# Performance work log

Measured on AMD Instinct MI355X. Metric: run time of the kernel, lower is better.

The kernel has to match this reference:

```python
import jax, jax.numpy as jnp
import numpy as np

D = 128      # embedding_dim
E = 50000    # positive edges per metapath
S = 16       # negative samples per edge
N_A = 100000 # nodes of type A (head type of both metapaths)
N_B = 50000  # nodes of type B (tail type of metapath 1)


def setup_inputs() -> dict:
    key = jax.random.key(0)
    ks = jax.random.split(key, 10)
    emb_A = jax.random.normal(ks[0], (N_A, D), dtype=jnp.float32)
    emb_B = jax.random.normal(ks[1], (N_B, D), dtype=jnp.float32)
    # nn.init.uniform_(a=-1, b=1)
    rel_emb = jax.random.uniform(ks[2], (2, D, D), dtype=jnp.float32, minval=-1.0, maxval=1.0)
    edge_index_m0 = jax.random.randint(ks[3], (2, E), 0, N_A)  # A -> A
    edge_index_m1 = jnp.stack([
        jax.random.randint(ks[4], (E,), 0, N_A),               # heads: type A
        jax.random.randint(ks[5], (E,), 0, N_B),               # tails: type B
    ])
    neg_head_m0 = jax.random.randint(ks[6], (E, S), 0, N_A)
    neg_head_m1 = jax.random.randint(ks[7], (E, S), 0, N_A)
    neg_tail_m0 = jax.random.randint(ks[8], (E, S), 0, N_A)
    neg_tail_m1 = jax.random.randint(ks[9], (E, S), 0, N_B)
    return dict(emb_A=emb_A, emb_B=emb_B, rel_emb=rel_emb,
                edge_index_m0=edge_index_m0, edge_index_m1=edge_index_m1,
                neg_head_m0=neg_head_m0, neg_head_m1=neg_head_m1,
                neg_tail_m0=neg_tail_m0, neg_tail_m1=neg_tail_m1)


# The torch module computes score = (A K B^T).sum(dim=1); summing the [E,E]
# score matrix over dim 1 equals contracting with sum_j b_j, so we never
# materialize the [E,E] (or [E*S, E*S]) matrix -- same math, fused reduction.

def _pos_score(K, emb_h, emb_t, edge_index):
    s = emb_t[edge_index[1]].sum(0)          # [d] = sum_j b_j
    return emb_h[edge_index[0]] @ (K @ s)    # [E]


def _neg_head_score(K, emb_h, neg):
    # predict(mode='head'): emb_A = emb_h[neg.reshape(-1)],
    # idx_B = edge_index[0][arange(E)*S] == neg[:, 0],
    # side_B = (K @ emb_h[idx_B].T).repeat_interleave(S, -1); sum over columns
    # == K @ (S * sum_j emb_h[neg[j, 0]]).
    s = neg.shape[1]
    c = K @ (s * emb_h[neg[:, 0]].sum(0))    # [d]
    return emb_h[neg.reshape(-1)] @ c        # [E*S]


def _neg_tail_score(K, emb_t, neg):
    # predict(mode='tail'): emb_B = emb_t[neg.reshape(-1)],
    # idx_A = edge_index[1][arange(E)*S] == neg[:, 0],
    # side_A = (emb_t[idx_A] @ K).repeat_interleave(S, 0); row sums of
    # side_A @ emb_B^T == side_A @ sum_j emb_B[j].
    s = neg.shape[1]
    sb = emb_t[neg.reshape(-1)].sum(0)       # [d]
    base = (emb_t[neg[:, 0]] @ K) @ sb       # [E]
    return jnp.repeat(base, s)               # [E*S]


def reference(emb_A, emb_B, rel_emb, edge_index_m0, edge_index_m1,
              neg_head_m0, neg_head_m1, neg_tail_m0, neg_tail_m1):
    K0, K1 = rel_emb[0], rel_emb[1]
    pos0 = _pos_score(K0, emb_A, emb_A, edge_index_m0)   # [E]
    pos1 = _pos_score(K1, emb_A, emb_B, edge_index_m1)   # [E]
    nh0 = _neg_head_score(K0, emb_A, neg_head_m0)        # [E*S]
    nh1 = _neg_head_score(K1, emb_A, neg_head_m1)        # [E*S]
    nt0 = _neg_tail_score(K0, emb_A, neg_tail_m0)        # [E*S]
    nt1 = _neg_tail_score(K1, emb_B, neg_tail_m1)        # [E*S]
    return jnp.concatenate([pos0, pos1, nh0, nh1, nt0, nt1])
```

## Files before the change

### kernel.cpp

```cpp
#include <hip/hip_runtime.h>
#include <stdint.h>

#define D 128
#define E_EDGES 50000
#define S_NEG 16
#define N_A 100000
#define N_B 50000
#define ES (E_EDGES * S_NEG)

#define HW 12500
#define ACH 38
#define BCH 34
#define GA 1024
#define GB 512
#define RPG 13
#define RA 32
#define RB 16

__device__ inline float dot4(float4 a, float4 b) {
    return a.x * b.x + a.y * b.y + a.z * b.z + a.w * b.w;
}
#define RED32(p) { p += __shfl_xor(p, 1); p += __shfl_xor(p, 2); p += __shfl_xor(p, 4); \
                   p += __shfl_xor(p, 8); p += __shfl_xor(p, 16); }


__global__ void k_hist(const int* __restrict__ ei0, const int* __restrict__ ei1,
                       const int* __restrict__ nh0, const int* __restrict__ nh1,
                       const int* __restrict__ nt0, const int* __restrict__ nt1,
                       uint32_t* __restrict__ partA, uint32_t* __restrict__ partB) {
    __shared__ uint32_t h[HW];
    const int tid = threadIdx.x;
    for (int w = tid; w < HW; w += 512) h[w] = 0;
    __syncthreads();

    const int b = blockIdx.x;
    if (b < 2 * ACH) {
        const int c = b >> 1, hh = b & 1;
        const unsigned lo = hh * 50000u;
        uint32_t* dst = partA + (size_t)b * HW;
        if (c >= 2 && c < 6) {
            const int* src = (c < 4) ? nh0 : nh1;
            const long long base = (long long)(c & 1) * 25000 * S_NEG;
            for (int i = tid; i < 25000; i += 512) {
                const unsigned r = (unsigned)src[base + (long long)i * S_NEG] - lo;
                if (r < 50000u) atomicAdd(&h[r >> 2], 1u << ((r & 3u) * 8u));
            }
        } else {
            const int* srcp = (c < 2) ? (ei0 + E_EDGES + c * 25000)
                                      : (nt0 + (c - 6) * 25000);
            const int4* src4 = reinterpret_cast<const int4*>(srcp);
            for (int i = tid; i < 6250; i += 512) {
                const int4 v = src4[i];
                unsigned r;
                r = (unsigned)v.x - lo; if (r < 50000u) atomicAdd(&h[r >> 2], 1u << ((r & 3u) * 8u));
                r = (unsigned)v.y - lo; if (r < 50000u) atomicAdd(&h[r >> 2], 1u << ((r & 3u) * 8u));
                r = (unsigned)v.z - lo; if (r < 50000u) atomicAdd(&h[r >> 2], 1u << ((r & 3u) * 8u));
                r = (unsigned)v.w - lo; if (r < 50000u) atomicAdd(&h[r >> 2], 1u << ((r & 3u) * 8u));
            }
        }
        __syncthreads();
        for (int w = tid; w < HW; w += 512) dst[w] = h[w];
    } else {
        const int c = b - 2 * ACH;
        uint32_t* dst = partB + (size_t)c * HW;
        const int* srcp = (c < 2) ? (ei1 + E_EDGES + c * 25000)
                                  : (nt1 + (c - 2) * 25000);
        const int4* src4 = reinterpret_cast<const int4*>(srcp);
        for (int i = tid; i < 6250; i += 512) {
            const int4 v = src4[i];
            unsigned r;
            r = (unsigned)v.x; if (r < 50000u) atomicAdd(&h[r >> 2], 1u << ((r & 3u) * 8u));
            r = (unsigned)v.y; if (r < 50000u) atomicAdd(&h[r >> 2], 1u << ((r & 3u) * 8u));
            r = (unsigned)v.z; if (r < 50000u) atomicAdd(&h[r >> 2], 1u << ((r & 3u) * 8u));
            r = (unsigned)v.w; if (r < 50000u) atomicAdd(&h[r >> 2], 1u << ((r & 3u) * 8u));
        }
        __syncthreads();
        for (int w = tid; w < HW; w += 512) dst[w] = h[w];
    }
}

__global__ void k_reduceC(const uint32_t* __restrict__ partA,
                          const uint32_t* __restrict__ partB,
                          float4* __restrict__ cwA, float2* __restrict__ cwB) {
    const int t = blockIdx.x * 256 + threadIdx.x;
    if (t < N_A) {
        const int n = t;
        const int hh = (n >= 50000);
        const int w = (n - hh * 50000) >> 2;
        const int sh = (n & 3) * 8;
        const uint32_t* p = partA + (size_t)hh * HW + w;
        unsigned s0 = 0, s1 = 0, s2 = 0, s3 = 0;
#pragma unroll
        for (int c = 0; c < 2; ++c)  s0 += (p[(size_t)(c * 2) * HW] >> sh) & 255u;
#pragma unroll
        for (int c = 2; c < 4; ++c)  s1 += (p[(size_t)(c * 2) * HW] >> sh) & 255u;
#pragma unroll
        for (int c = 4; c < 6; ++c)  s2 += (p[(size_t)(c * 2) * HW] >> sh) & 255u;
#pragma unroll 8
        for (int c = 6; c < 38; ++c) s3 += (p[(size_t)(c * 2) * HW] >> sh) & 255u;
        cwA[n] = make_float4((float)s0, (float)s1, (float)s2, (float)s3);
    } else if (t < N_A + N_B) {
        const int n = t - N_A;
        const int w = n >> 2;
        const int sh = (n & 3) * 8;
        const uint32_t* p = partB + w;
        unsigned s0 = 0, s1 = 0;
#pragma unroll
        for (int c = 0; c < 2; ++c)  s0 += (p[(size_t)c * HW] >> sh) & 255u;
#pragma unroll 8
        for (int c = 2; c < 34; ++c) s1 += (p[(size_t)c * HW] >> sh) & 255u;
        cwB[n] = make_float2((float)s0, (float)s1);
    }
}

__global__ void k_scan1(const float* __restrict__ embA, const float* __restrict__ embB,
                        const float4* __restrict__ cwA, const float2* __restrict__ cwB,
                        float* __restrict__ psumA, float* __restrict__ psumB) {
    __shared__ float sds[4 * D];
    const int tid = threadIdx.x;
    const int l = tid & 31;
    const int grp = tid >> 5;

    for (int j = tid; j < 4 * D; j += 256) sds[j] = 0.f;
    __syncthreads();

    if ((int)blockIdx.x < GA) {
        const int gid = blockIdx.x * 8 + grp;
        int r = gid * RPG;
        const int end = min(r + RPG, N_A);
        float acc[16];
#pragma unroll
        for (int k = 0; k < 16; ++k) acc[k] = 0.f;
        const float* base = embA + 4 * l;
        for (; r + 4 <= end; r += 4) {
            float4 w[4], x[4];
#pragma unroll
            for (int u = 0; u < 4; ++u) w[u] = cwA[r + u];
#pragma unroll
            for (int u = 0; u < 4; ++u)
                x[u] = *reinterpret_cast<const float4*>(base + (size_t)(r + u) * D);
#pragma unroll
            for (int u = 0; u < 4; ++u) {
                acc[0]  += w[u].x * x[u].x; acc[1]  += w[u].x * x[u].y;
                acc[2]  += w[u].x * x[u].z; acc[3]  += w[u].x * x[u].w;
                acc[4]  += w[u].y * x[u].x; acc[5]  += w[u].y * x[u].y;
                acc[6]  += w[u].y * x[u].z; acc[7]  += w[u].y * x[u].w;
                acc[8]  += w[u].z * x[u].x; acc[9]  += w[u].z * x[u].y;
                acc[10] += w[u].z * x[u].z; acc[11] += w[u].z * x[u].w;
                acc[12] += w[u].w * x[u].x; acc[13] += w[u].w * x[u].y;
                acc[14] += w[u].w * x[u].z; acc[15] += w[u].w * x[u].w;
            }
        }
        for (; r < end; ++r) {
            const float4 w0 = cwA[r];
            const float4 x0 = *reinterpret_cast<const float4*>(base + (size_t)r * D);
            acc[0]  += w0.x * x0.x; acc[1]  += w0.x * x0.y; acc[2]  += w0.x * x0.z; acc[3]  += w0.x * x0.w;
            acc[4]  += w0.y * x0.x; acc[5]  += w0.y * x0.y; acc[6]  += w0.y * x0.z; acc[7]  += w0.y * x0.w;
            acc[8]  += w0.z * x0.x; acc[9]  += w0.z * x0.y; acc[10] += w0.z * x0.z; acc[11] += w0.z * x0.w;
            acc[12] += w0.w * x0.x; acc[13] += w0.w * x0.y; acc[14] += w0.w * x0.z; acc[15] += w0.w * x0.w;
        }
#pragma unroll
        for (int p = 0; p < 4; ++p)
#pragma unroll
            for (int k = 0; k < 4; ++k)
                atomicAdd(&sds[p * D + 4 * l + k], acc[p * 4 + k]);
        __syncthreads();
        for (int j = tid; j < 4 * D; j += 256)
            psumA[(size_t)blockIdx.x * 512 + j] = sds[j];
    } else {
        const int gid = (blockIdx.x - GA) * 8 + grp;
        int r = gid * RPG;
        const int end = min(r + RPG, N_B);
        float acc[8];
#pragma unroll
        for (int k = 0; k < 8; ++k) acc[k] = 0.f;
        const float* base = embB + 4 * l;
        for (; r + 4 <= end; r += 4) {
            float2 w[4]; float4 x[4];
#pragma unroll
            for (int u = 0; u < 4; ++u) w[u] = cwB[r + u];
#pragma unroll
            for (int u = 0; u < 4; ++u)
                x[u] = *reinterpret_cast<const float4*>(base + (size_t)(r + u) * D);
#pragma unroll
            for (int u = 0; u < 4; ++u) {
                acc[0] += w[u].x * x[u].x; acc[1] += w[u].x * x[u].y;
                acc[2] += w[u].x * x[u].z; acc[3] += w[u].x * x[u].w;
                acc[4] += w[u].y * x[u].x; acc[5] += w[u].y * x[u].y;
                acc[6] += w[u].y * x[u].z; acc[7] += w[u].y * x[u].w;
            }
        }
        for (; r < end; ++r) {
            const float2 w0 = cwB[r];
            const float4 x0 = *reinterpret_cast<const float4*>(base + (size_t)r * D);
            acc[0] += w0.x * x0.x; acc[1] += w0.x * x0.y; acc[2] += w0.x * x0.z; acc[3] += w0.x * x0.w;
            acc[4] += w0.y * x0.x; acc[5] += w0.y * x0.y; acc[6] += w0.y * x0.z; acc[7] += w0.y * x0.w;
        }
#pragma unroll
        for (int p = 0; p < 2; ++p)
#pragma unroll
            for (int k = 0; k < 4; ++k)
                atomicAdd(&sds[p * D + 4 * l + k], acc[p * 4 + k]);
        __syncthreads();
        for (int j = tid; j < 2 * D; j += 256)
            psumB[(size_t)(blockIdx.x - GA) * 256 + j] = sds[j];
    }
}

__global__ void k_red1(const float* __restrict__ psumA, const float* __restrict__ psumB,
                       float* __restrict__ psumA2, float* __restrict__ psumB2) {
    const int b = blockIdx.x, t = threadIdx.x;
    if (b < RA) {
        const float* p = psumA + (size_t)b * 32 * 512;
        float s0 = 0.f, s1 = 0.f;
#pragma unroll 8
        for (int r = 0; r < 32; ++r) { s0 += p[r * 512 + t]; s1 += p[r * 512 + 256 + t]; }
        psumA2[(size_t)b * 512 + t] = s0;
        psumA2[(size_t)b * 512 + 256 + t] = s1;
    } else {
        const int bi = b - RA;
        const float* p = psumB + (size_t)bi * 32 * 256;
        float s = 0.f;
#pragma unroll 8
        for (int r = 0; r < 32; ++r) s += p[r * 256 + t];
        psumB2[(size_t)bi * 256 + t] = s;
    }
}

__global__ void k_cvec2(const float* __restrict__ rel,
                        const float* __restrict__ psumA2, const float* __restrict__ psumB2,
                        float* __restrict__ cvec) {
    const int j = blockIdx.x;
    const int tid = threadIdx.x;
    __shared__ float Kds[D * 129];
    __shared__ float red[256];
    __shared__ float sv[D];
    const float* Kp = rel + (size_t)(j & 1) * D * D;

    for (int e = tid; e < D * D / 4; e += 256) {
        const int row = e >> 5, col = (e & 31) * 4;
        const float4 v = *reinterpret_cast<const float4*>(Kp + (size_t)row * D + col);
        float* dst = Kds + row * 129 + col;
        dst[0] = v.x; dst[1] = v.y; dst[2] = v.z; dst[3] = v.w;
    }

    const int g = tid >> 7, i = tid & 127;
    float s = 0.f;
    if (j == 1 || j == 5) {
        const int plane = (j == 1) ? 0 : 1;
        for (int b = g; b < RB; b += 2) s += psumB2[(size_t)b * 256 + plane * D + i];
    } else {
        const int plane = (j == 0) ? 0 : (j - 1);
        for (int b = g; b < RA; b += 2) s += psumA2[(size_t)b * 512 + plane * D + i];
    }
    red[tid] = s;
    __syncthreads();
    if (tid < 128) sv[i] = red[i] + red[128 + i];
    __syncthreads();

    if (tid < 128) {
        const float scale = (j == 2 || j == 3) ? (float)S_NEG : 1.0f;
        float acc = 0.f;
#pragma unroll
        for (int k = 0; k < D; k += 4)
            acc += Kds[i * 129 + k] * sv[k] + Kds[i * 129 + k + 1] * sv[k + 1]
                 + Kds[i * 129 + k + 2] * sv[k + 2] + Kds[i * 129 + k + 3] * sv[k + 3];
        cvec[j * D + i] = acc * scale;
    }
}

__global__ void k_scan2(const float* __restrict__ embA, const float* __restrict__ embB,
                        const float* __restrict__ cvec, float* __restrict__ PA,
                        float* __restrict__ PB) {
    __shared__ float sc[5 * D];
    const int tid = threadIdx.x;
    const int l = tid & 31;
    const int grp = tid >> 5;

    if ((int)blockIdx.x < GA) {
        for (int j = tid; j < 5 * D; j += 256) sc[j] = cvec[j];
        __syncthreads();
        float4 cf[5];
#pragma unroll
        for (int p = 0; p < 5; ++p)
            cf[p] = *reinterpret_cast<const float4*>(sc + p * D + 4 * l);
        const int gid = blockIdx.x * 8 + grp;
        int r = gid * RPG;
        const int end = min(r + RPG, N_A);
        const float* base = embA + 4 * l;
        for (; r + 4 <= end; r += 4) {
            float4 x[4];
#pragma unroll
            for (int u = 0; u < 4; ++u)
                x[u] = *reinterpret_cast<const float4*>(base + (size_t)(r + u) * D);
            float p_[4][5];
#pragma unroll
            for (int u = 0; u < 4; ++u)
#pragma unroll
                for (int p = 0; p < 5; ++p) p_[u][p] = dot4(x[u], cf[p]);
#pragma unroll
            for (int u = 0; u < 4; ++u)
#pragma unroll
                for (int p = 0; p < 5; ++p) RED32(p_[u][p]);
            if (l < 4) {
#pragma unroll
                for (int p = 0; p < 5; ++p) {
                    float v = p_[0][p];
                    v = (l == 1) ? p_[1][p] : v;
                    v = (l == 2) ? p_[2][p] : v;
                    v = (l == 3) ? p_[3][p] : v;
                    PA[(size_t)p * N_A + r + l] = v;
                }
            }
        }
        for (; r < end; ++r) {
            const float4 x0 = *reinterpret_cast<const float4*>(base + (size_t)r * D);
            float q[5];
#pragma unroll
            for (int p = 0; p < 5; ++p) { q[p] = dot4(x0, cf[p]); RED32(q[p]); }
            if (l == 0) {
#pragma unroll
                for (int p = 0; p < 5; ++p) PA[(size_t)p * N_A + r] = q[p];
            }
        }
    } else {
        for (int j = tid; j < D; j += 256) sc[j] = cvec[5 * D + j];
        __syncthreads();
        const float4 cf = *reinterpret_cast<const float4*>(sc + 4 * l);
        const int gid = (blockIdx.x - GA) * 8 + grp;
        int r = gid * RPG;
        const int end = min(r + RPG, N_B);
        const float* base = embB + 4 * l;
        for (; r + 4 <= end; r += 4) {
            float4 x[4];
#pragma unroll
            for (int u = 0; u < 4; ++u)
                x[u] = *reinterpret_cast<const float4*>(base + (size_t)(r + u) * D);
            float p_[4];
#pragma unroll
            for (int u = 0; u < 4; ++u) { p_[u] = dot4(x[u], cf); RED32(p_[u]); }
            if (l < 4)
                PB[r + l] = (l == 1) ? p_[1] : (l == 2) ? p_[2] : (l == 3) ? p_[3] : p_[0];
        }
        for (; r < end; ++r) {
            const float4 x0 = *reinterpret_cast<const float4*>(base + (size_t)r * D);
            float q = dot4(x0, cf); RED32(q);
            if (l == 0) PB[r] = q;
        }
    }
}

__global__ void k_scatter(const int* __restrict__ ei0, const int* __restrict__ ei1,
                          const int* __restrict__ nh0, const int* __restrict__ nh1,
                          const int* __restrict__ nt0, const int* __restrict__ nt1,
                          const float* __restrict__ PA, const float* __restrict__ PB,
                          float* __restrict__ out) {
    const int total4 = (2 * E_EDGES + 4 * ES) / 4;
    const float* P0 = PA;
    const float* P1 = PA + (size_t)N_A;
    const float* P2 = PA + (size_t)2 * N_A;
    const float* P3 = PA + (size_t)3 * N_A;
    const float* P4 = PA + (size_t)4 * N_A;
    for (int t = blockIdx.x * blockDim.x + threadIdx.x; t < total4;
         t += gridDim.x * blockDim.x) {
        const int e = t * 4;
        float4 v;
        if (e < E_EDGES) {
            const int4 i4 = *reinterpret_cast<const int4*>(ei0 + e);
            v = make_float4(P0[i4.x], P0[i4.y], P0[i4.z], P0[i4.w]);
        } else if (e < 2 * E_EDGES) {
            const int4 i4 = *reinterpret_cast<const int4*>(ei1 + (e - E_EDGES));
            v = make_float4(P1[i4.x], P1[i4.y], P1[i4.z], P1[i4.w]);
        } else if (e < 2 * E_EDGES + ES) {
            const int4 i4 = *reinterpret_cast<const int4*>(nh0 + (e - 2 * E_EDGES));
            v = make_float4(P2[i4.x], P2[i4.y], P2[i4.z], P2[i4.w]);
        } else if (e < 2 * E_EDGES + 2 * ES) {
            const int4 i4 = *reinterpret_cast<const int4*>(nh1 + (e - 2 * E_EDGES - ES));
            v = make_float4(P3[i4.x], P3[i4.y], P3[i4.z], P3[i4.w]);
        } else if (e < 2 * E_EDGES + 3 * ES) {
            const int i = e - 2 * E_EDGES - 2 * ES;
            const float s = P4[nt0[(i >> 4) << 4]];
            v = make_float4(s, s, s, s);
        } else {
            const int i = e - 2 * E_EDGES - 3 * ES;
            const float s = PB[nt1[(i >> 4) << 4]];
            v = make_float4(s, s, s, s);
        }
        *reinterpret_cast<float4*>(out + e) = v;
    }
}

extern "C" void kernel_launch(void* const* d_in, const int* in_sizes, int n_in,
                              void* d_out, int out_size, void* d_ws, size_t ws_size,
                              hipStream_t stream) {
    const float* embA = (const float*)d_in[0];
    const float* embB = (const float*)d_in[1];
    const float* rel  = (const float*)d_in[2];
    const int* ei0 = (const int*)d_in[3];
    const int* ei1 = (const int*)d_in[4];
    const int* nh0 = (const int*)d_in[5];
    const int* nh1 = (const int*)d_in[6];
    const int* nt0 = (const int*)d_in[7];
    const int* nt1 = (const int*)d_in[8];
    float* out = (float*)d_out;

    uint32_t* partA = (uint32_t*)d_ws;
    uint32_t* partB = partA + (size_t)2 * ACH * HW;
    float4* cwA = (float4*)(partB + (size_t)BCH * HW);
    float2* cwB = (float2*)(cwA + N_A);
    float* psumA = (float*)(cwB + N_B);
    float* psumB = psumA + (size_t)GA * 512;
    float* psumA2 = psumB + (size_t)GB * 256;
    float* psumB2 = psumA2 + (size_t)RA * 512;
    float* cvec  = psumB2 + (size_t)RB * 256;
    float* PA    = cvec + 6 * D;
    float* PB    = PA + (size_t)5 * N_A;

    k_hist<<<2 * ACH + BCH, 512, 0, stream>>>(ei0, ei1, nh0, nh1, nt0, nt1, partA, partB);
    k_reduceC<<<(N_A + N_B + 255) / 256, 256, 0, stream>>>(partA, partB, cwA, cwB);
    k_scan1<<<GA + GB, 256, 0, stream>>>(embA, embB, cwA, cwB, psumA, psumB);
    k_red1<<<RA + RB, 256, 0, stream>>>(psumA, psumB, psumA2, psumB2);
    k_cvec2<<<6, 256, 0, stream>>>(rel, psumA2, psumB2, cvec);
    k_scan2<<<GA + GB, 256, 0, stream>>>(embA, embB, cvec, PA, PB);
    k_scatter<<<2048, 256, 0, stream>>>(ei0, ei1, nh0, nh1, nt0, nt1, PA, PB, out);
}
```

Baseline: 227.4 us.

## Restructure embedding scans: exact row partitioning, prefetching, thread-per-row projection

```diff
diff --git a/kernel.cpp b/kernel.cpp
--- a/kernel.cpp
+++ b/kernel.cpp
@@ -11,17 +11,28 @@
 #define HW 12500
 #define ACH 38
 #define BCH 34
-#define GA 1024
-#define GB 512
-#define RPG 13
-#define RA 32
-#define RB 16
+
+#define GA1 500
+#define GB1 250
+#define RPG 25
+#define RA2 20
+#define RB2 10
+#define GA2 391
+#define GB2 196
 
 __device__ inline float dot4(float4 a, float4 b) {
     return a.x * b.x + a.y * b.y + a.z * b.z + a.w * b.w;
 }
-#define RED32(p) { p += __shfl_xor(p, 1); p += __shfl_xor(p, 2); p += __shfl_xor(p, 4); \
-                   p += __shfl_xor(p, 8); p += __shfl_xor(p, 16); }
+__device__ inline void fma16(float* acc, const float4 w, const float4 x) {
+    acc[0]  += w.x * x.x; acc[1]  += w.x * x.y; acc[2]  += w.x * x.z; acc[3]  += w.x * x.w;
+    acc[4]  += w.y * x.x; acc[5]  += w.y * x.y; acc[6]  += w.y * x.z; acc[7]  += w.y * x.w;
+    acc[8]  += w.z * x.x; acc[9]  += w.z * x.y; acc[10] += w.z * x.z; acc[11] += w.z * x.w;
+    acc[12] += w.w * x.x; acc[13] += w.w * x.y; acc[14] += w.w * x.z; acc[15] += w.w * x.w;
+}
+__device__ inline void fma8(float* acc, const float2 w, const float4 x) {
+    acc[0] += w.x * x.x; acc[1] += w.x * x.y; acc[2] += w.x * x.z; acc[3] += w.x * x.w;
+    acc[4] += w.y * x.x; acc[5] += w.y * x.y; acc[6] += w.y * x.z; acc[7] += w.y * x.w;
+}
 
 
 __global__ void k_hist(const int* __restrict__ ei0, const int* __restrict__ ei1,
@@ -113,116 +124,121 @@
     }
 }
 
-__global__ void k_scan1(const float* __restrict__ embA, const float* __restrict__ embB,
-                        const float4* __restrict__ cwA, const float2* __restrict__ cwB,
-                        float* __restrict__ psumA, float* __restrict__ psumB) {
-    __shared__ float sds[4 * D];
+__global__ void __launch_bounds__(256, 4)
+k_scan1(const float* __restrict__ embA, const float* __restrict__ embB,
+        const float4* __restrict__ cwA, const float2* __restrict__ cwB,
+        float* __restrict__ psumA, float* __restrict__ psumB) {
+    __shared__ float sds[4 * 512];
     const int tid = threadIdx.x;
     const int l = tid & 31;
     const int grp = tid >> 5;
-
-    for (int j = tid; j < 4 * D; j += 256) sds[j] = 0.f;
-    __syncthreads();
-
-    if ((int)blockIdx.x < GA) {
-        const int gid = blockIdx.x * 8 + grp;
-        int r = gid * RPG;
-        const int end = min(r + RPG, N_A);
+    const int wid = tid >> 6;
+
+    if ((int)blockIdx.x < GA1) {
+        const int r0 = (blockIdx.x * 8 + grp) * RPG;
+        const float* base = embA + 4 * l;
         float acc[16];
 #pragma unroll
         for (int k = 0; k < 16; ++k) acc[k] = 0.f;
-        const float* base = embA + 4 * l;
-        for (; r + 4 <= end; r += 4) {
-            float4 w[4], x[4];
-#pragma unroll
-            for (int u = 0; u < 4; ++u) w[u] = cwA[r + u];
-#pragma unroll
-            for (int u = 0; u < 4; ++u)
-                x[u] = *reinterpret_cast<const float4*>(base + (size_t)(r + u) * D);
-#pragma unroll
-            for (int u = 0; u < 4; ++u) {
-                acc[0]  += w[u].x * x[u].x; acc[1]  += w[u].x * x[u].y;
-                acc[2]  += w[u].x * x[u].z; acc[3]  += w[u].x * x[u].w;
-                acc[4]  += w[u].y * x[u].x; acc[5]  += w[u].y * x[u].y;
-                acc[6]  += w[u].y * x[u].z; acc[7]  += w[u].y * x[u].w;
-                acc[8]  += w[u].z * x[u].x; acc[9]  += w[u].z * x[u].y;
-                acc[10] += w[u].z * x[u].z; acc[11] += w[u].z * x[u].w;
-                acc[12] += w[u].w * x[u].x; acc[13] += w[u].w * x[u].y;
-                acc[14] += w[u].w * x[u].z; acc[15] += w[u].w * x[u].w;
-            }
-        }
-        for (; r < end; ++r) {
-            const float4 w0 = cwA[r];
-            const float4 x0 = *reinterpret_cast<const float4*>(base + (size_t)r * D);
-            acc[0]  += w0.x * x0.x; acc[1]  += w0.x * x0.y; acc[2]  += w0.x * x0.z; acc[3]  += w0.x * x0.w;
-            acc[4]  += w0.y * x0.x; acc[5]  += w0.y * x0.y; acc[6]  += w0.y * x0.z; acc[7]  += w0.y * x0.w;
-            acc[8]  += w0.z * x0.x; acc[9]  += w0.z * x0.y; acc[10] += w0.z * x0.z; acc[11] += w0.z * x0.w;
-            acc[12] += w0.w * x0.x; acc[13] += w0.w * x0.y; acc[14] += w0.w * x0.z; acc[15] += w0.w * x0.w;
-        }
-#pragma unroll
-        for (int p = 0; p < 4; ++p)
-#pragma unroll
-            for (int k = 0; k < 4; ++k)
-                atomicAdd(&sds[p * D + 4 * l + k], acc[p * 4 + k]);
-        __syncthreads();
-        for (int j = tid; j < 4 * D; j += 256)
-            psumA[(size_t)blockIdx.x * 512 + j] = sds[j];
+        float4 wc[5], xc[5];
+#pragma unroll
+        for (int u = 0; u < 5; ++u) {
+            wc[u] = cwA[r0 + u];
+            xc[u] = *reinterpret_cast<const float4*>(base + (size_t)(r0 + u) * D);
+        }
+#pragma unroll
+        for (int b = 0; b < 5; ++b) {
+            float4 wn[5], xn[5];
+            if (b < 4) {
+#pragma unroll
+                for (int u = 0; u < 5; ++u) {
+                    const int rr = r0 + (b + 1) * 5 + u;
+                    wn[u] = cwA[rr];
+                    xn[u] = *reinterpret_cast<const float4*>(base + (size_t)rr * D);
+                }
+            }
+#pragma unroll
+            for (int u = 0; u < 5; ++u) fma16(acc, wc[u], xc[u]);
+            if (b < 4) {
+#pragma unroll
+                for (int u = 0; u < 5; ++u) { wc[u] = wn[u]; xc[u] = xn[u]; }
+            }
+        }
+#pragma unroll
+        for (int k = 0; k < 16; ++k) acc[k] += __shfl_xor(acc[k], 32);
+        if ((tid & 32) == 0) {
+            float* w0 = sds + wid * 512;
+#pragma unroll
+            for (int p = 0; p < 4; ++p)
+                *reinterpret_cast<float4*>(w0 + p * 128 + 4 * l) =
+                    make_float4(acc[4 * p], acc[4 * p + 1], acc[4 * p + 2], acc[4 * p + 3]);
+        }
+        __syncthreads();
+        for (int j = tid; j < 512; j += 256)
+            psumA[(size_t)blockIdx.x * 512 + j] =
+                sds[j] + sds[512 + j] + sds[1024 + j] + sds[1536 + j];
     } else {
-        const int gid = (blockIdx.x - GA) * 8 + grp;
-        int r = gid * RPG;
-        const int end = min(r + RPG, N_B);
+        const int r0 = ((blockIdx.x - GA1) * 8 + grp) * RPG;
+        const float* base = embB + 4 * l;
         float acc[8];
 #pragma unroll
         for (int k = 0; k < 8; ++k) acc[k] = 0.f;
-        const float* base = embB + 4 * l;
-        for (; r + 4 <= end; r += 4) {
-            float2 w[4]; float4 x[4];
-#pragma unroll
-            for (int u = 0; u < 4; ++u) w[u] = cwB[r + u];
-#pragma unroll
-            for (int u = 0; u < 4; ++u)
-                x[u] = *reinterpret_cast<const float4*>(base + (size_t)(r + u) * D);
-#pragma unroll
-            for (int u = 0; u < 4; ++u) {
-                acc[0] += w[u].x * x[u].x; acc[1] += w[u].x * x[u].y;
-                acc[2] += w[u].x * x[u].z; acc[3] += w[u].x * x[u].w;
-                acc[4] += w[u].y * x[u].x; acc[5] += w[u].y * x[u].y;
-                acc[6] += w[u].y * x[u].z; acc[7] += w[u].y * x[u].w;
-            }
-        }
-        for (; r < end; ++r) {
-            const float2 w0 = cwB[r];
-            const float4 x0 = *reinterpret_cast<const float4*>(base + (size_t)r * D);
-            acc[0] += w0.x * x0.x; acc[1] += w0.x * x0.y; acc[2] += w0.x * x0.z; acc[3] += w0.x * x0.w;
-            acc[4] += w0.y * x0.x; acc[5] += w0.y * x0.y; acc[6] += w0.y * x0.z; acc[7] += w0.y * x0.w;
-        }
-#pragma unroll
-        for (int p = 0; p < 2; ++p)
-#pragma unroll
-            for (int k = 0; k < 4; ++k)
-                atomicAdd(&sds[p * D + 4 * l + k], acc[p * 4 + k]);
-        __syncthreads();
-        for (int j = tid; j < 2 * D; j += 256)
-            psumB[(size_t)(blockIdx.x - GA) * 256 + j] = sds[j];
+        float2 wc[5]; float4 xc[5];
+#pragma unroll
+        for (int u = 0; u < 5; ++u) {
+            wc[u] = cwB[r0 + u];
+            xc[u] = *reinterpret_cast<const float4*>(base + (size_t)(r0 + u) * D);
+        }
+#pragma unroll
+        for (int b = 0; b < 5; ++b) {
+            float2 wn[5]; float4 xn[5];
+            if (b < 4) {
+#pragma unroll
+                for (int u = 0; u < 5; ++u) {
+                    const int rr = r0 + (b + 1) * 5 + u;
+                    wn[u] = cwB[rr];
+                    xn[u] = *reinterpret_cast<const float4*>(base + (size_t)rr * D);
+                }
+            }
+#pragma unroll
+            for (int u = 0; u < 5; ++u) fma8(acc, wc[u], xc[u]);
+            if (b < 4) {
+#pragma unroll
+                for (int u = 0; u < 5; ++u) { wc[u] = wn[u]; xc[u] = xn[u]; }
+            }
+        }
+#pragma unroll
+        for (int k = 0; k < 8; ++k) acc[k] += __shfl_xor(acc[k], 32);
+        if ((tid & 32) == 0) {
+            float* w0 = sds + wid * 256;
+#pragma unroll
+            for (int p = 0; p < 2; ++p)
+                *reinterpret_cast<float4*>(w0 + p * 128 + 4 * l) =
+                    make_float4(acc[4 * p], acc[4 * p + 1], acc[4 * p + 2], acc[4 * p + 3]);
+        }
+        __syncthreads();
+        for (int j = tid; j < 256; j += 256)
+            psumB[(size_t)(blockIdx.x - GA1) * 256 + j] =
+                sds[j] + sds[256 + j] + sds[512 + j] + sds[768 + j];
     }
 }
 
 __global__ void k_red1(const float* __restrict__ psumA, const float* __restrict__ psumB,
                        float* __restrict__ psumA2, float* __restrict__ psumB2) {
     const int b = blockIdx.x, t = threadIdx.x;
-    if (b < RA) {
-        const float* p = psumA + (size_t)b * 32 * 512;
+    if (b < RA2) {
+        const float* p = psumA + (size_t)b * 25 * 512;
         float s0 = 0.f, s1 = 0.f;
-#pragma unroll 8
-        for (int r = 0; r < 32; ++r) { s0 += p[r * 512 + t]; s1 += p[r * 512 + 256 + t]; }
+#pragma unroll 5
+        for (int r = 0; r < 25; ++r) { s0 += p[r * 512 + t]; s1 += p[r * 512 + 256 + t]; }
         psumA2[(size_t)b * 512 + t] = s0;
         psumA2[(size_t)b * 512 + 256 + t] = s1;
     } else {
-        const int bi = b - RA;
-        const float* p = psumB + (size_t)bi * 32 * 256;
+        const int bi = b - RA2;
+        const float* p = psumB + (size_t)bi * 25 * 256;
         float s = 0.f;
-#pragma unroll 8
-        for (int r = 0; r < 32; ++r) s += p[r * 256 + t];
+#pragma unroll 5
+        for (int r = 0; r < 25; ++r) s += p[r * 256 + t];
         psumB2[(size_t)bi * 256 + t] = s;
     }
 }
@@ -248,10 +264,10 @@
     float s = 0.f;
     if (j == 1 || j == 5) {
         const int plane = (j == 1) ? 0 : 1;
-        for (int b = g; b < RB; b += 2) s += psumB2[(size_t)b * 256 + plane * D + i];
+        for (int b = g; b < RB2; b += 2) s += psumB2[(size_t)b * 256 + plane * D + i];
     } else {
         const int plane = (j == 0) ? 0 : (j - 1);
-        for (int b = g; b < RA; b += 2) s += psumA2[(size_t)b * 512 + plane * D + i];
+        for (int b = g; b < RA2; b += 2) s += psumA2[(size_t)b * 512 + plane * D + i];
     }
     red[tid] = s;
     __syncthreads();
@@ -269,84 +285,49 @@
     }
 }
 
-__global__ void k_scan2(const float* __restrict__ embA, const float* __restrict__ embB,
-                        const float* __restrict__ cvec, float* __restrict__ PA,
-                        float* __restrict__ PB) {
+__global__ void __launch_bounds__(256, 4)
+k_scan2(const float* __restrict__ embA, const float* __restrict__ embB,
+        const float* __restrict__ cvec, float* __restrict__ PA,
+        float* __restrict__ PB) {
     __shared__ float sc[5 * D];
     const int tid = threadIdx.x;
-    const int l = tid & 31;
-    const int grp = tid >> 5;
-
-    if ((int)blockIdx.x < GA) {
+
+    if ((int)blockIdx.x < GA2) {
         for (int j = tid; j < 5 * D; j += 256) sc[j] = cvec[j];
         __syncthreads();
-        float4 cf[5];
-#pragma unroll
-        for (int p = 0; p < 5; ++p)
-            cf[p] = *reinterpret_cast<const float4*>(sc + p * D + 4 * l);
-        const int gid = blockIdx.x * 8 + grp;
-        int r = gid * RPG;
-        const int end = min(r + RPG, N_A);
-        const float* base = embA + 4 * l;
-        for (; r + 4 <= end; r += 4) {
-            float4 x[4];
-#pragma unroll
-            for (int u = 0; u < 4; ++u)
-                x[u] = *reinterpret_cast<const float4*>(base + (size_t)(r + u) * D);
-            float p_[4][5];
-#pragma unroll
-            for (int u = 0; u < 4; ++u)
-#pragma unroll
-                for (int p = 0; p < 5; ++p) p_[u][p] = dot4(x[u], cf[p]);
-#pragma unroll
-            for (int u = 0; u < 4; ++u)
-#pragma unroll
-                for (int p = 0; p < 5; ++p) RED32(p_[u][p]);
-            if (l < 4) {
-#pragma unroll
-                for (int p = 0; p < 5; ++p) {
-                    float v = p_[0][p];
-                    v = (l == 1) ? p_[1][p] : v;
-                    v = (l == 2) ? p_[2][p] : v;
-                    v = (l == 3) ? p_[3][p] : v;
-                    PA[(size_t)p * N_A + r + l] = v;
-                }
-            }
-        }
-        for (; r < end; ++r) {
-            const float4 x0 = *reinterpret_cast<const float4*>(base + (size_t)r * D);
-            float q[5];
-#pragma unroll
-            for (int p = 0; p < 5; ++p) { q[p] = dot4(x0, cf[p]); RED32(q[p]); }
-            if (l == 0) {
-#pragma unroll
-                for (int p = 0; p < 5; ++p) PA[(size_t)p * N_A + r] = q[p];
-            }
+        const int n = blockIdx.x * 256 + tid;
+        const int nc = min(n, N_A - 1);
+        const float4* row = reinterpret_cast<const float4*>(embA + (size_t)nc * D);
+        float a0 = 0.f, a1 = 0.f, a2 = 0.f, a3 = 0.f, a4 = 0.f;
+#pragma unroll 8
+        for (int k = 0; k < 32; ++k) {
+            const float4 x = row[k];
+            a0 += dot4(x, *reinterpret_cast<const float4*>(sc + 0 * D + 4 * k));
+            a1 += dot4(x, *reinterpret_cast<const float4*>(sc + 1 * D + 4 * k));
+            a2 += dot4(x, *reinterpret_cast<const float4*>(sc + 2 * D + 4 * k));
+            a3 += dot4(x, *reinterpret_cast<const float4*>(sc + 3 * D + 4 * k));
+            a4 += dot4(x, *reinterpret_cast<const float4*>(sc + 4 * D + 4 * k));
+        }
+        if (n < N_A) {
+            PA[0 * (size_t)N_A + n] = a0;
+            PA[1 * (size_t)N_A + n] = a1;
+            PA[2 * (size_t)N_A + n] = a2;
+            PA[3 * (size_t)N_A + n] = a3;
+            PA[4 * (size_t)N_A + n] = a4;
         }
     } else {
         for (int j = tid; j < D; j += 256) sc[j] = cvec[5 * D + j];
         __syncthreads();
-        const float4 cf = *reinterpret_cast<const float4*>(sc + 4 * l);
-        const int gid = (blockIdx.x - GA) * 8 + grp;
-        int r = gid * RPG;
-        const int end = min(r + RPG, N_B);
-        const float* base = embB + 4 * l;
-        for (; r + 4 <= end; r += 4) {
-            float4 x[4];
-#pragma unroll
-            for (int u = 0; u < 4; ++u)
-                x[u] = *reinterpret_cast<const float4*>(base + (size_t)(r + u) * D);
-            float p_[4];
-#pragma unroll
-            for (int u = 0; u < 4; ++u) { p_[u] = dot4(x[u], cf); RED32(p_[u]); }
-            if (l < 4)
-                PB[r + l] = (l == 1) ? p_[1] : (l == 2) ? p_[2] : (l == 3) ? p_[3] : p_[0];
-        }
-        for (; r < end; ++r) {
-            const float4 x0 = *reinterpret_cast<const float4*>(base + (size_t)r * D);
-            float q = dot4(x0, cf); RED32(q);
-            if (l == 0) PB[r] = q;
-        }
+        const int n = (blockIdx.x - GA2) * 256 + tid;
+        const int nc = min(n, N_B - 1);
+        const float4* row = reinterpret_cast<const float4*>(embB + (size_t)nc * D);
+        float a0 = 0.f;
+#pragma unroll 8
+        for (int k = 0; k < 32; ++k) {
+            const float4 x = row[k];
+            a0 += dot4(x, *reinterpret_cast<const float4*>(sc + 4 * k));
+        }
+        if (n < N_B) PB[n] = a0;
     }
 }
 
@@ -409,18 +390,18 @@
     float4* cwA = (float4*)(partB + (size_t)BCH * HW);
     float2* cwB = (float2*)(cwA + N_A);
     float* psumA = (float*)(cwB + N_B);
-    float* psumB = psumA + (size_t)GA * 512;
-    float* psumA2 = psumB + (size_t)GB * 256;
-    float* psumB2 = psumA2 + (size_t)RA * 512;
-    float* cvec  = psumB2 + (size_t)RB * 256;
+    float* psumB = psumA + (size_t)GA1 * 512;
+    float* psumA2 = psumB + (size_t)GB1 * 256;
+    float* psumB2 = psumA2 + (size_t)RA2 * 512;
+    float* cvec  = psumB2 + (size_t)RB2 * 256;
     float* PA    = cvec + 6 * D;
     float* PB    = PA + (size_t)5 * N_A;
 
     k_hist<<<2 * ACH + BCH, 512, 0, stream>>>(ei0, ei1, nh0, nh1, nt0, nt1, partA, partB);
     k_reduceC<<<(N_A + N_B + 255) / 256, 256, 0, stream>>>(partA, partB, cwA, cwB);
-    k_scan1<<<GA + GB, 256, 0, stream>>>(embA, embB, cwA, cwB, psumA, psumB);
-    k_red1<<<RA + RB, 256, 0, stream>>>(psumA, psumB, psumA2, psumB2);
+    k_scan1<<<GA1 + GB1, 256, 0, stream>>>(embA, embB, cwA, cwB, psumA, psumB);
+    k_red1<<<RA2 + RB2, 256, 0, stream>>>(psumA, psumB, psumA2, psumB2);
     k_cvec2<<<6, 256, 0, stream>>>(rel, psumA2, psumB2, cvec);
-    k_scan2<<<GA + GB, 256, 0, stream>>>(embA, embB, cvec, PA, PB);
+    k_scan2<<<GA2 + GB2, 256, 0, stream>>>(embA, embB, cvec, PA, PB);
     k_scatter<<<2048, 256, 0, stream>>>(ei0, ei1, nh0, nh1, nt0, nt1, PA, PB, out);
 }
```

Result: faster. 191.4 us (-15.9%).
